# Performance work log

Hardware: AMD Instinct MI355X
Metric: run time of the kernel (lower is better)

The kernel has to match this reference:

```python
import jax, jax.numpy as jnp
import numpy as np

H = 512   # hidden_size
IN = 5    # input_size
OUT = 2   # output_size
B = 2048
T_HIST = 50


def _lstm_cell(x, h, c, W_ih, W_hh, b_ih, b_hh):
    # PyTorch gate order: i, f, g, o
    z = x @ W_ih.T + h @ W_hh.T + (b_ih + b_hh)
    i, f, g, o = jnp.split(z, 4, axis=-1)
    i = jax.nn.sigmoid(i)
    f = jax.nn.sigmoid(f)
    g = jnp.tanh(g)
    o = jax.nn.sigmoid(o)
    c2 = f * c + i * g
    h2 = o * jnp.tanh(c2)
    return h2, c2


def setup_inputs() -> dict:
    key = jax.random.key(0)
    ks = jax.random.split(key, 20)
    s = 0.05
    inp = {
        "history": jax.random.normal(ks[0], (B, T_HIST, IN), dtype=jnp.float32),
        "future_frames": 30,
        # encoder layer 0 (input IN) and layer 1 (input H)
        "enc_W_ih0": jax.random.normal(ks[1], (4 * H, IN)) * s,
        "enc_W_hh0": jax.random.normal(ks[2], (4 * H, H)) * s,
        "enc_b_ih0": jnp.zeros((4 * H,), jnp.float32),
        "enc_b_hh0": jnp.zeros((4 * H,), jnp.float32),
        "enc_W_ih1": jax.random.normal(ks[3], (4 * H, H)) * s,
        "enc_W_hh1": jax.random.normal(ks[4], (4 * H, H)) * s,
        "enc_b_ih1": jnp.zeros((4 * H,), jnp.float32),
        "enc_b_hh1": jnp.zeros((4 * H,), jnp.float32),
        # decoder layer 0 (input OUT) and layer 1 (input H)
        "dec_W_ih0": jax.random.normal(ks[5], (4 * H, OUT)) * s,
        "dec_W_hh0": jax.random.normal(ks[6], (4 * H, H)) * s,
        "dec_b_ih0": jnp.zeros((4 * H,), jnp.float32),
        "dec_b_hh0": jnp.zeros((4 * H,), jnp.float32),
        "dec_W_ih1": jax.random.normal(ks[7], (4 * H, H)) * s,
        "dec_W_hh1": jax.random.normal(ks[8], (4 * H, H)) * s,
        "dec_b_ih1": jnp.zeros((4 * H,), jnp.float32),
        "dec_b_hh1": jnp.zeros((4 * H,), jnp.float32),
        # output head
        "out_W": jax.random.normal(ks[9], (OUT, H)) * s,
        "out_b": jnp.zeros((OUT,), jnp.float32),
    }
    return inp


def reference(history, enc_W_ih0, enc_W_hh0, enc_b_ih0, enc_b_hh0,
              enc_W_ih1, enc_W_hh1, enc_b_ih1, enc_b_hh1,
              dec_W_ih0, dec_W_hh0, dec_b_ih0, dec_b_hh0,
              dec_W_ih1, dec_W_hh1, dec_b_ih1, dec_b_hh1,
              out_W, out_b, future_frames):
    batch = history.shape[0]
    z = jnp.zeros((batch, H), history.dtype)

    # ----- encoder: 2-layer LSTM over history, scan over time -----
    def enc_step(carry, x_t):
        h0, c0, h1, c1 = carry
        h0, c0 = _lstm_cell(x_t, h0, c0, enc_W_ih0, enc_W_hh0, enc_b_ih0, enc_b_hh0)
        h1, c1 = _lstm_cell(h0, h1, c1, enc_W_ih1, enc_W_hh1, enc_b_ih1, enc_b_hh1)
        return (h0, c0, h1, c1), None

    xs = jnp.swapaxes(history, 0, 1)  # [T, B, IN]
    (h0, c0, h1, c1), _ = jax.lax.scan(enc_step, (z, z, z, z), xs)

    def dec_step(carry, _):
        h0, c0, h1, c1, x_prev = carry
        h0, c0 = _lstm_cell(x_prev, h0, c0, dec_W_ih0, dec_W_hh0, dec_b_ih0, dec_b_hh0)
        h1, c1 = _lstm_cell(h0, h1, c1, dec_W_ih1, dec_W_hh1, dec_b_ih1, dec_b_hh1)
        pred = h1 @ out_W.T + out_b  # [B, OUT]
        return (h0, c0, h1, c1, pred), pred

    x0 = jnp.zeros((batch, OUT), history.dtype)
    _, preds = jax.lax.scan(dec_step, (h0, c0, h1, c1, x0), None, length=future_frames)
    return jnp.swapaxes(preds, 0, 1)  # [B, T_fut, OUT]
```

## Files before the change

kernel.cpp:

```cpp
#include <hip/hip_runtime.h>
#include <hip/hip_bf16.h>


#define HDIM 512
#define BDIM 2048
#define T_HIST 50
#define T_FUT 30

typedef __attribute__((ext_vector_type(8))) short short8;
typedef __attribute__((ext_vector_type(4))) float f32x4;

#define AS1(p) ((const __attribute__((address_space(1))) void*)(p))
#define AS3(p) ((__attribute__((address_space(3))) void*)(p))

__device__ __forceinline__ ushort f2bf(float f) {
    union { float f; unsigned u; } v; v.f = f;
    unsigned r = v.u + 0x7fff + ((v.u >> 16) & 1);
    return (ushort)(r >> 16);
}
__device__ __forceinline__ float bf2f(ushort h) {
    union { unsigned u; float f; } v; v.u = ((unsigned)h) << 16;
    return v.f;
}

struct SplitSrc { const float* src[6]; };

__global__ __launch_bounds__(256) void split_weights(SplitSrc s, ushort* __restrict__ hi,
                                                     ushort* __restrict__ lo) {
    int row = blockIdx.x;
    int j = blockIdx.y;
    int g = row >> 9, u = row & 511;
    int rp = (u >> 5) * 128 + ((u >> 4) & 1) * 64 + g * 16 + (u & 15);
    const float* S = s.src[j] + (size_t)row * HDIM;
    ushort* H = hi + ((size_t)j * 2048 + rp) * HDIM;
    ushort* L = lo + ((size_t)j * 2048 + rp) * HDIM;
    for (int k = threadIdx.x; k < HDIM; k += 256) {
        float w = S[k];
        ushort hb = f2bf(w);
        H[k] = hb;
        L[k] = f2bf(w - bf2f(hb));
    }
}

__global__ __launch_bounds__(256) void lstm_cell_mfma(
    const ushort* __restrict__ A1hi, const ushort* __restrict__ A1lo,
    const ushort* __restrict__ W1hi, const ushort* __restrict__ W1lo,
    const ushort* __restrict__ A2hi, const ushort* __restrict__ A2lo,
    const ushort* __restrict__ W2hi, const ushort* __restrict__ W2lo,
    int np,
    const float* __restrict__ x, int x_stride, int Kx, const float* __restrict__ Wx,
    const float* __restrict__ bih, const float* __restrict__ bhh,
    float* __restrict__ c_state, ushort* __restrict__ h_hi, ushort* __restrict__ h_lo)
{
    __shared__ __align__(16) ushort lds[2][32768];

    const int tid = threadIdx.x;
    const int w = tid >> 6, l = tid & 63;
    const int wm = w >> 1, wn = w & 1;
    const int lrow = l & 15, lk = l >> 4;

    int id = blockIdx.y * 16 + blockIdx.x;
    int xcd = id & 7, rr = id >> 3;
    int bx = (xcd & 3) * 4 + (rr & 3);
    int by = (xcd >> 2) * 8 + (rr >> 2);
    const int m0 = by * 128;
    const int n0 = bx * 128;
    const int u  = bx * 32 + wn * 16 + lrow;

    f32x4 acc[4][4];

    auto STAGE = [&](int buf, int t) {
        int p = t >> 3;
        int kc = (t & 7) * 64;
        const ushort* Ah = p ? A2hi : A1hi;
        const ushort* Al = p ? A2lo : A1lo;
        const ushort* Bh = p ? W2hi : W1hi;
        const ushort* Bl = p ? W2lo : W1lo;
        ushort* base = &lds[buf][0];
        #pragma unroll
        for (int it = 0; it < 4; ++it) {
            int sb = (w * 4 + it) * 64;
            int slot = sb + l;
            int row = slot >> 3;
            int spx = (slot & 7) ^ (row & 7);
            size_t go = (size_t)row * HDIM + kc + spx * 8;
            __builtin_amdgcn_global_load_lds(AS1(Ah + (size_t)m0 * HDIM + go),
                                             AS3(base + sb * 8), 16, 0, 0);
            __builtin_amdgcn_global_load_lds(AS1(Al + (size_t)m0 * HDIM + go),
                                             AS3(base + 8192 + sb * 8), 16, 0, 0);
            __builtin_amdgcn_global_load_lds(AS1(Bh + (size_t)n0 * HDIM + go),
                                             AS3(base + 16384 + sb * 8), 16, 0, 0);
            __builtin_amdgcn_global_load_lds(AS1(Bl + (size_t)n0 * HDIM + go),
                                             AS3(base + 24576 + sb * 8), 16, 0, 0);
        }
    };

    STAGE(0, 0);

    #pragma unroll
    for (int g = 0; g < 4; ++g) {
        float b = bih[g * HDIM + u] + bhh[g * HDIM + u];
        f32x4 bv = {b, b, b, b};
        #pragma unroll
        for (int fm = 0; fm < 4; ++fm) acc[fm][g] = bv;
    }

    if (Kx > 0) {
        for (int kx = 0; kx < Kx; ++kx) {
            float wv[4];
            #pragma unroll
            for (int g = 0; g < 4; ++g) wv[g] = Wx[(size_t)(g * HDIM + u) * Kx + kx];
            #pragma unroll
            for (int fm = 0; fm < 4; ++fm)
                #pragma unroll
                for (int r = 0; r < 4; ++r) {
                    int m = m0 + wm * 64 + fm * 16 + lk * 4 + r;
                    float xv = x[(size_t)m * x_stride + kx];
                    #pragma unroll
                    for (int g = 0; g < 4; ++g) acc[fm][g][r] += xv * wv[g];
                }
        }
    }

    const int nch = np * 8;
    for (int t = 0; t < nch; ++t) {
        int cur = t & 1;
        __syncthreads();
        if (t + 1 < nch) STAGE(cur ^ 1, t + 1);
        ushort* base = &lds[cur][0];
        #pragma unroll
        for (int ks = 0; ks < 2; ++ks) {
            short8 ah[4], al[4], bh[4], bl[4];
            #pragma unroll
            for (int fm = 0; fm < 4; ++fm) {
                int row = wm * 64 + fm * 16 + lrow;
                int spx = (ks * 4 + lk) ^ (row & 7);
                int off = (row * 8 + spx) * 8;
                ah[fm] = *(const short8*)(base + off);
                al[fm] = *(const short8*)(base + 8192 + off);
            }
            #pragma unroll
            for (int g = 0; g < 4; ++g) {
                int row = wn * 64 + g * 16 + lrow;
                int spx = (ks * 4 + lk) ^ (row & 7);
                int off = (row * 8 + spx) * 8;
                bh[g] = *(const short8*)(base + 16384 + off);
                bl[g] = *(const short8*)(base + 24576 + off);
            }
            #pragma unroll
            for (int fm = 0; fm < 4; ++fm)
                #pragma unroll
                for (int g = 0; g < 4; ++g)
                    acc[fm][g] = __builtin_amdgcn_mfma_f32_16x16x32_bf16(
                        ah[fm], bh[g], acc[fm][g], 0, 0, 0);
            #pragma unroll
            for (int fm = 0; fm < 4; ++fm)
                #pragma unroll
                for (int g = 0; g < 4; ++g)
                    acc[fm][g] = __builtin_amdgcn_mfma_f32_16x16x32_bf16(
                        al[fm], bh[g], acc[fm][g], 0, 0, 0);
            #pragma unroll
            for (int fm = 0; fm < 4; ++fm)
                #pragma unroll
                for (int g = 0; g < 4; ++g)
                    acc[fm][g] = __builtin_amdgcn_mfma_f32_16x16x32_bf16(
                        ah[fm], bl[g], acc[fm][g], 0, 0, 0);
        }
    }

    #pragma unroll
    for (int fm = 0; fm < 4; ++fm)
        #pragma unroll
        for (int r = 0; r < 4; ++r) {
            int m = m0 + wm * 64 + fm * 16 + lk * 4 + r;
            size_t idx = (size_t)m * HDIM + u;
            float zi = acc[fm][0][r], zf = acc[fm][1][r];
            float zg = acc[fm][2][r], zo = acc[fm][3][r];
            float ig = 1.f / (1.f + __expf(-zi));
            float fg = 1.f / (1.f + __expf(-zf));
            float gg = 2.f / (1.f + __expf(-2.f * zg)) - 1.f;
            float og = 1.f / (1.f + __expf(-zo));
            float cn = fg * c_state[idx] + ig * gg;
            float hn = og * (2.f / (1.f + __expf(-2.f * cn)) - 1.f);
            c_state[idx] = cn;
            ushort hb = f2bf(hn);
            h_hi[idx] = hb;
            h_lo[idx] = f2bf(hn - bf2f(hb));
        }
}

__global__ __launch_bounds__(256) void head_kernel(
    const ushort* __restrict__ hhi, const ushort* __restrict__ hlo,
    const float* __restrict__ Wout, const float* __restrict__ bout,
    float* __restrict__ out, float* __restrict__ xbuf, int t)
{
    int wave = (blockIdx.x * 256 + threadIdx.x) >> 6;
    int lane = threadIdx.x & 63;
    const ushort* hr = hhi + (size_t)wave * HDIM;
    const ushort* lr = hlo + (size_t)wave * HDIM;
    float s0 = 0.f, s1 = 0.f;
    #pragma unroll
    for (int k = lane; k < HDIM; k += 64) {
        float hv = bf2f(hr[k]) + bf2f(lr[k]);
        s0 += hv * Wout[k];
        s1 += hv * Wout[HDIM + k];
    }
    #pragma unroll
    for (int off = 32; off > 0; off >>= 1) {
        s0 += __shfl_down(s0, off);
        s1 += __shfl_down(s1, off);
    }
    if (lane == 0) {
        float p0 = s0 + bout[0], p1 = s1 + bout[1];
        out[(size_t)wave * (T_FUT * 2) + t * 2 + 0] = p0;
        out[(size_t)wave * (T_FUT * 2) + t * 2 + 1] = p1;
        xbuf[wave * 2 + 0] = p0;
        xbuf[wave * 2 + 1] = p1;
    }
}

extern "C" void kernel_launch(void* const* d_in, const int* in_sizes, int n_in,
                              void* d_out, int out_size, void* d_ws, size_t ws_size,
                              hipStream_t stream) {
    const float* history = (const float*)d_in[0];
    const float* eWih0 = (const float*)d_in[2];
    const float* eWhh0 = (const float*)d_in[3];
    const float* ebih0 = (const float*)d_in[4];
    const float* ebhh0 = (const float*)d_in[5];
    const float* eWih1 = (const float*)d_in[6];
    const float* eWhh1 = (const float*)d_in[7];
    const float* ebih1 = (const float*)d_in[8];
    const float* ebhh1 = (const float*)d_in[9];
    const float* dWih0 = (const float*)d_in[10];
    const float* dWhh0 = (const float*)d_in[11];
    const float* dbih0 = (const float*)d_in[12];
    const float* dbhh0 = (const float*)d_in[13];
    const float* dWih1 = (const float*)d_in[14];
    const float* dWhh1 = (const float*)d_in[15];
    const float* dbih1 = (const float*)d_in[16];
    const float* dbhh1 = (const float*)d_in[17];
    const float* outW  = (const float*)d_in[18];
    const float* outb  = (const float*)d_in[19];
    float* out = (float*)d_out;

    const size_t M = (size_t)2048 * 512;
    ushort* whi = (ushort*)d_ws;
    ushort* wlo = whi + 6 * M;
    ushort* hb  = wlo + 6 * M;
    float*  c0  = (float*)(hb + 8 * M);
    float*  c1  = c0 + M;
    float*  xbuf = c1 + M;

    ushort* h0a_hi = hb + 0 * M; ushort* h0a_lo = hb + 1 * M;
    ushort* h0b_hi = hb + 2 * M; ushort* h0b_lo = hb + 3 * M;
    ushort* h1a_hi = hb + 4 * M; ushort* h1a_lo = hb + 5 * M;
    ushort* h1b_hi = hb + 6 * M; ushort* h1b_lo = hb + 7 * M;

    hipMemsetAsync(h0a_hi, 0, 2 * M * sizeof(ushort), stream);
    hipMemsetAsync(h1a_hi, 0, 2 * M * sizeof(ushort), stream);
    hipMemsetAsync(c0, 0, 2 * M * sizeof(float), stream);
    hipMemsetAsync(xbuf, 0, BDIM * 2 * sizeof(float), stream);

    SplitSrc ss;
    ss.src[0] = eWhh0; ss.src[1] = eWih1; ss.src[2] = eWhh1;
    ss.src[3] = dWhh0; ss.src[4] = dWih1; ss.src[5] = dWhh1;
    split_weights<<<dim3(2048, 6), 256, 0, stream>>>(ss, whi, wlo);

    #define WHI(j) (whi + (size_t)(j) * M)
    #define WLO(j) (wlo + (size_t)(j) * M)

    dim3 cgrid(16, 16);
    dim3 blk(256);

    for (int s = 0; s < T_HIST + T_FUT; ++s) {
        ushort* h0r_hi = (s & 1) ? h0b_hi : h0a_hi;
        ushort* h0r_lo = (s & 1) ? h0b_lo : h0a_lo;
        ushort* h0w_hi = (s & 1) ? h0a_hi : h0b_hi;
        ushort* h0w_lo = (s & 1) ? h0a_lo : h0b_lo;
        ushort* h1r_hi = (s & 1) ? h1b_hi : h1a_hi;
        ushort* h1r_lo = (s & 1) ? h1b_lo : h1a_lo;
        ushort* h1w_hi = (s & 1) ? h1a_hi : h1b_hi;
        ushort* h1w_lo = (s & 1) ? h1a_lo : h1b_lo;

        if (s < T_HIST) {
            lstm_cell_mfma<<<cgrid, blk, 0, stream>>>(
                h0r_hi, h0r_lo, WHI(0), WLO(0),
                nullptr, nullptr, nullptr, nullptr, 1,
                history + s * 5, T_HIST * 5, 5, eWih0,
                ebih0, ebhh0, c0, h0w_hi, h0w_lo);
            lstm_cell_mfma<<<cgrid, blk, 0, stream>>>(
                h0w_hi, h0w_lo, WHI(1), WLO(1),
                h1r_hi, h1r_lo, WHI(2), WLO(2), 2,
                nullptr, 0, 0, nullptr,
                ebih1, ebhh1, c1, h1w_hi, h1w_lo);
        } else {
            lstm_cell_mfma<<<cgrid, blk, 0, stream>>>(
                h0r_hi, h0r_lo, WHI(3), WLO(3),
                nullptr, nullptr, nullptr, nullptr, 1,
                xbuf, 2, 2, dWih0,
                dbih0, dbhh0, c0, h0w_hi, h0w_lo);
            lstm_cell_mfma<<<cgrid, blk, 0, stream>>>(
                h0w_hi, h0w_lo, WHI(4), WLO(4),
                h1r_hi, h1r_lo, WHI(5), WLO(5), 2,
                nullptr, 0, 0, nullptr,
                dbih1, dbhh1, c1, h1w_hi, h1w_lo);
            head_kernel<<<512, blk, 0, stream>>>(h1w_hi, h1w_lo, outW, outb,
                                                 out, xbuf, s - T_HIST);
        }
    }
    #undef WHI
    #undef WLO
}
```

Measured before the change: 3.966 ms.

## Deepen LDS pipeline to four K=32 stages with explicit vmcnt waits

Replaces the double-buffered K=64 staging with a 4-slot ring of K=32 chunks, prefetching two chunks ahead. The old __syncthreads is replaced by explicit s_waitcnt vmcnt counts plus s_barrier, which keeps more global-to-LDS loads in flight and hides load latency better. A new XOR swizzle fits the narrower row layout. The risks are more barriers per unit of K, which halves the MFMA work between syncs, and a tight dependence on the hardcoded vmcnt values being correct.

```diff
diff --git a/kernel.cpp b/kernel.cpp
--- a/kernel.cpp
+++ b/kernel.cpp
@@ -21,6 +21,12 @@
 __device__ __forceinline__ float bf2f(ushort h) {
     union { unsigned u; float f; } v; v.u = ((unsigned)h) << 16;
     return v.f;
+}
+
+__device__ __forceinline__ int swz(int row, int slot) {
+    int q = row >> 1;
+    int t = ((row & 1) << 2) | slot;
+    return q * 8 + (t ^ (q & 7));
 }
 
 struct SplitSrc { const float* src[6]; };
@@ -52,7 +58,7 @@
     const float* __restrict__ bih, const float* __restrict__ bhh,
     float* __restrict__ c_state, ushort* __restrict__ h_hi, ushort* __restrict__ h_lo)
 {
-    __shared__ __align__(16) ushort lds[2][32768];
+    __shared__ __align__(16) ushort lds[4 * 16384];
 
     const int tid = threadIdx.x;
     const int w = tid >> 6, l = tid & 63;
@@ -69,34 +75,6 @@
 
     f32x4 acc[4][4];
 
-    auto STAGE = [&](int buf, int t) {
-        int p = t >> 3;
-        int kc = (t & 7) * 64;
-        const ushort* Ah = p ? A2hi : A1hi;
-        const ushort* Al = p ? A2lo : A1lo;
-        const ushort* Bh = p ? W2hi : W1hi;
-        const ushort* Bl = p ? W2lo : W1lo;
-        ushort* base = &lds[buf][0];
-        #pragma unroll
-        for (int it = 0; it < 4; ++it) {
-            int sb = (w * 4 + it) * 64;
-            int slot = sb + l;
-            int row = slot >> 3;
-            int spx = (slot & 7) ^ (row & 7);
-            size_t go = (size_t)row * HDIM + kc + spx * 8;
-            __builtin_amdgcn_global_load_lds(AS1(Ah + (size_t)m0 * HDIM + go),
-                                             AS3(base + sb * 8), 16, 0, 0);
-            __builtin_amdgcn_global_load_lds(AS1(Al + (size_t)m0 * HDIM + go),
-                                             AS3(base + 8192 + sb * 8), 16, 0, 0);
-            __builtin_amdgcn_global_load_lds(AS1(Bh + (size_t)n0 * HDIM + go),
-                                             AS3(base + 16384 + sb * 8), 16, 0, 0);
-            __builtin_amdgcn_global_load_lds(AS1(Bl + (size_t)n0 * HDIM + go),
-                                             AS3(base + 24576 + sb * 8), 16, 0, 0);
-        }
-    };
-
-    STAGE(0, 0);
-
     #pragma unroll
     for (int g = 0; g < 4; ++g) {
         float b = bih[g * HDIM + u] + bhh[g * HDIM + u];
@@ -104,7 +82,6 @@
         #pragma unroll
         for (int fm = 0; fm < 4; ++fm) acc[fm][g] = bv;
     }
-
     if (Kx > 0) {
         for (int kx = 0; kx < Kx; ++kx) {
             float wv[4];
@@ -122,50 +99,85 @@
         }
     }
 
-    const int nch = np * 8;
+    auto STAGE = [&](int t) {
+        int buf = t & 3;
+        int p = t >> 4;
+        int kc = (t & 15) * 32;
+        const ushort* Ah = p ? A2hi : A1hi;
+        const ushort* Al = p ? A2lo : A1lo;
+        const ushort* Bh = p ? W2hi : W1hi;
+        const ushort* Bl = p ? W2lo : W1lo;
+        ushort* base = &lds[buf * 16384];
+        #pragma unroll
+        for (int it = 0; it < 2; ++it) {
+            int db = (w * 2 + it) * 64;
+            int d = db + l;
+            int q = d >> 3, tp = d & 7;
+            int tl = tp ^ (q & 7);
+            int r = (q << 1) | (tl >> 2);
+            int s = tl & 3;
+            size_t go = (size_t)r * HDIM + kc + s * 8;
+            __builtin_amdgcn_global_load_lds(AS1(Ah + (size_t)m0 * HDIM + go),
+                                             AS3(base + db * 8), 16, 0, 0);
+            __builtin_amdgcn_global_load_lds(AS1(Al + (size_t)m0 * HDIM + go),
+                                             AS3(base + 4096 + db * 8), 16, 0, 0);
+            __builtin_amdgcn_global_load_lds(AS1(Bh + (size_t)n0 * HDIM + go),
+                                             AS3(base + 8192 + db * 8), 16, 0, 0);
+            __builtin_amdgcn_global_load_lds(AS1(Bl + (size_t)n0 * HDIM + go),
+                                             AS3(base + 12288 + db * 8), 16, 0, 0);
+        }
+    };
+
+    const int nch = np * 16;
+    STAGE(0);
+    STAGE(1);
+
     for (int t = 0; t < nch; ++t) {
-        int cur = t & 1;
-        __syncthreads();
-        if (t + 1 < nch) STAGE(cur ^ 1, t + 1);
-        ushort* base = &lds[cur][0];
-        #pragma unroll
-        for (int ks = 0; ks < 2; ++ks) {
-            short8 ah[4], al[4], bh[4], bl[4];
-            #pragma unroll
-            for (int fm = 0; fm < 4; ++fm) {
-                int row = wm * 64 + fm * 16 + lrow;
-                int spx = (ks * 4 + lk) ^ (row & 7);
-                int off = (row * 8 + spx) * 8;
-                ah[fm] = *(const short8*)(base + off);
-                al[fm] = *(const short8*)(base + 8192 + off);
-            }
-            #pragma unroll
-            for (int g = 0; g < 4; ++g) {
-                int row = wn * 64 + g * 16 + lrow;
-                int spx = (ks * 4 + lk) ^ (row & 7);
-                int off = (row * 8 + spx) * 8;
-                bh[g] = *(const short8*)(base + 16384 + off);
-                bl[g] = *(const short8*)(base + 24576 + off);
-            }
-            #pragma unroll
-            for (int fm = 0; fm < 4; ++fm)
-                #pragma unroll
-                for (int g = 0; g < 4; ++g)
-                    acc[fm][g] = __builtin_amdgcn_mfma_f32_16x16x32_bf16(
-                        ah[fm], bh[g], acc[fm][g], 0, 0, 0);
-            #pragma unroll
-            for (int fm = 0; fm < 4; ++fm)
-                #pragma unroll
-                for (int g = 0; g < 4; ++g)
-                    acc[fm][g] = __builtin_amdgcn_mfma_f32_16x16x32_bf16(
-                        al[fm], bh[g], acc[fm][g], 0, 0, 0);
-            #pragma unroll
-            for (int fm = 0; fm < 4; ++fm)
-                #pragma unroll
-                for (int g = 0; g < 4; ++g)
-                    acc[fm][g] = __builtin_amdgcn_mfma_f32_16x16x32_bf16(
-                        ah[fm], bl[g], acc[fm][g], 0, 0, 0);
-        }
+        if (t + 2 < nch) {
+            STAGE(t + 2);
+            asm volatile("s_waitcnt vmcnt(16)" ::: "memory");
+        } else if (t + 1 < nch) {
+            asm volatile("s_waitcnt vmcnt(8)" ::: "memory");
+        } else {
+            asm volatile("s_waitcnt vmcnt(0)" ::: "memory");
+        }
+        __builtin_amdgcn_s_barrier();
+        __builtin_amdgcn_sched_barrier(0);
+
+        ushort* base = &lds[(t & 3) * 16384];
+        short8 ah[4], al[4], bh[4], bl[4];
+        #pragma unroll
+        for (int fm = 0; fm < 4; ++fm) {
+            int row = wm * 64 + fm * 16 + lrow;
+            int off = swz(row, lk) * 8;
+            ah[fm] = *(const short8*)(base + off);
+            al[fm] = *(const short8*)(base + 4096 + off);
+        }
+        #pragma unroll
+        for (int g = 0; g < 4; ++g) {
+            int row = wn * 64 + g * 16 + lrow;
+            int off = swz(row, lk) * 8;
+            bh[g] = *(const short8*)(base + 8192 + off);
+            bl[g] = *(const short8*)(base + 12288 + off);
+        }
+        #pragma unroll
+        for (int fm = 0; fm < 4; ++fm)
+            #pragma unroll
+            for (int g = 0; g < 4; ++g)
+                acc[fm][g] = __builtin_amdgcn_mfma_f32_16x16x32_bf16(
+                    ah[fm], bh[g], acc[fm][g], 0, 0, 0);
+        #pragma unroll
+        for (int fm = 0; fm < 4; ++fm)
+            #pragma unroll
+            for (int g = 0; g < 4; ++g)
+                acc[fm][g] = __builtin_amdgcn_mfma_f32_16x16x32_bf16(
+                    al[fm], bh[g], acc[fm][g], 0, 0, 0);
+        #pragma unroll
+        for (int fm = 0; fm < 4; ++fm)
+            #pragma unroll
+            for (int g = 0; g < 4; ++g)
+                acc[fm][g] = __builtin_amdgcn_mfma_f32_16x16x32_bf16(
+                    ah[fm], bl[g], acc[fm][g], 0, 0, 0);
     }
 
     #pragma unroll
```

New measurement: 4.140 ms. 1.04x slower.
